# Kernel tuning notes

Measured on AMD Instinct MI355X. Metric: run time of the kernel, lower is better.

## Reference

```python
import jax, jax.numpy as jnp
import numpy as np

TOPK = 5    # top-k nearest neighbours for the loss
TOPKP = 10  # top-k' for the constraint mask


def _normalize(x):
    # matches torch F.normalize(dim=1) for well-conditioned random inputs
    return x / jnp.linalg.norm(x, axis=1, keepdims=True)


def setup_inputs() -> dict:
    key = jax.random.key(0)
    ks = jax.random.split(key, 9)
    B, D, K, N = 256, 512, 128000, 100000
    queue = _normalize(jax.random.normal(ks[2], (K, D), jnp.float32))  # init normalizes queue
    return {
        "query": jax.random.normal(ks[0], (B, D), jnp.float32),
        "current_target": jax.random.normal(ks[1], (B, D), jnp.float32),
        "queue": queue,
        "pool": jax.random.normal(ks[3], (2, N, D), jnp.float32),
        "labels_bank": jax.random.randint(ks[4], (B * 0 + K,), 0, 1000, dtype=jnp.int32).astype(jnp.int64) if False else jax.random.randint(ks[4], (K,), 0, 1000),
        "index_queue": jax.random.randint(ks[5], (K,), 0, N),
        "pool_qindex": jax.random.randint(ks[6], (N,), 0, 2),
        "labels": jax.random.randint(ks[7], (B,), 0, 1000),
        "indices": jax.random.randint(ks[8], (B,), 0, N),
    }


def reference(query, current_target, queue, pool, labels_bank, index_queue,
              pool_qindex, labels, indices):
    B = query.shape[0]
    q = _normalize(query)                                   # [B, D]
    # target branch is under torch.no_grad(); queue/pool are detached buffers
    t = jax.lax.stop_gradient(_normalize(current_target))   # [B, D]
    queue = jax.lax.stop_gradient(queue)
    pool = jax.lax.stop_gradient(pool)

    # --- _dequeue_and_enqueue with queue_ptr = 0 ---
    pool = pool.at[pool_qindex[indices], indices].set(t)
    pool_qindex = pool_qindex.at[indices].set((pool_qindex[indices] + 1) % 2)
    queue = queue.at[:B].set(t)
    labels_bank = labels_bank.at[:B].set(labels)
    index_queue = index_queue.at[:B].set(indices)

    # --- cdist (squared L2 of unit vectors) against the 128k bank ---
    dist_t = 2.0 - 2.0 * jnp.einsum('bc,kc->bk', t, queue)  # [B, K]
    dist_q = 2.0 - 2.0 * jnp.einsum('bc,kc->bk', q, queue)  # [B, K]

    # unconstrained NN: smallest distances == largest -dist
    _, un_idx = jax.lax.top_k(-dist_t, TOPK)                # [B, TOPK]
    nn_q_un = jnp.take_along_axis(dist_q, un_idx, axis=1)

    # --- constraint branch on the epoch pool ---
    targets_prime = pool[pool_qindex[index_queue], index_queue]  # [K, D]
    ct_prime = pool[pool_qindex[indices], indices]               # [B, D]
    dist_tp = 2.0 - 2.0 * jnp.einsum('bc,kc->bk', ct_prime, targets_prime)
    _, idx_p = jax.lax.top_k(-dist_tp, TOPKP)                    # [B, TOPKP]

    # scatter -5 at constrained positions (topk indices are unique, so add == set)
    dist_t = dist_t.at[jnp.arange(B)[:, None], idx_p].add(-5.0)

    _, con_idx = jax.lax.top_k(-dist_t, TOPK)
    nn_q_con = jnp.take_along_axis(dist_q, con_idx, axis=1)

    loss = ((nn_q_con.sum(axis=1) / TOPK).mean()
            + (nn_q_un.sum(axis=1) / TOPK).mean()) / 2.0

    matches = (labels_bank[un_idx] == labels[:, None]).astype(jnp.float32)
    purity = (matches.sum(axis=1) / TOPK).mean()
    return loss, purity
```

## Files before the change

### kernel.cpp

```cpp
#include <hip/hip_runtime.h>
#include <math.h>

#define B_SZ 256
#define D_SZ 512
#define K_SZ 128000
#define N_SZ 100000

#define OFF_T     0UL
#define OFF_Q     524288UL
#define OFF_TH    1048576UL
#define OFF_CTH   1310720UL
#define OFF_NPQ   1572864UL
#define OFF_TPROW 1973248UL
#define OFF_UN    2485248UL
#define OFF_IDXP  2490880UL
#define OFF_SC    2501632UL

typedef __attribute__((ext_vector_type(4))) float    f32x4;
typedef __attribute__((ext_vector_type(8))) _Float16 f16x8;

__device__ __forceinline__ float block_sum(float v, float* red) {
  #pragma unroll
  for (int o = 32; o > 0; o >>= 1) v += __shfl_down(v, o, 64);
  const int w = threadIdx.x >> 6;
  const int l = threadIdx.x & 63;
  __syncthreads();
  if (l == 0) red[w] = v;
  __syncthreads();
  return red[0] + red[1] + red[2] + red[3];
}

__global__ __launch_bounds__(256) void prep_rows_kernel(
    const float* __restrict__ query, const float* __restrict__ ctar,
    const float* __restrict__ pool, const int* __restrict__ pool_qindex,
    const int* __restrict__ indices,
    float* __restrict__ t_f32, float* __restrict__ q_f32,
    _Float16* __restrict__ t_f16, _Float16* __restrict__ ct_f16)
{
  __shared__ float red[4];
  const int b = blockIdx.x, tid = threadIdx.x;
  const long base = (long)b * D_SZ;
  float x0 = query[base + tid], x1 = query[base + 256 + tid];
  float y0 = ctar[base + tid],  y1 = ctar[base + 256 + tid];
  float sq = block_sum(x0 * x0 + x1 * x1, red);
  float st = block_sum(y0 * y0 + y1 * y1, red);
  float rq = 1.f / sqrtf(sq);
  float rt = 1.f / sqrtf(st);
  q_f32[base + tid] = x0 * rq; q_f32[base + 256 + tid] = x1 * rq;
  float t0 = y0 * rt, t1 = y1 * rt;
  t_f32[base + tid] = t0; t_f32[base + 256 + tid] = t1;
  t_f16[base + tid] = (_Float16)t0; t_f16[base + 256 + tid] = (_Float16)t1;
  int i = indices[b];
  int slot = 1 - pool_qindex[i];
  const float* pr = pool + ((long)slot * N_SZ + i) * D_SZ;
  ct_f16[base + tid] = (_Float16)pr[tid];
  ct_f16[base + 256 + tid] = (_Float16)pr[tid + 256];
}

__global__ void prep_newpq_kernel(const int* __restrict__ pq, int* __restrict__ new_pq) {
  int i = blockIdx.x * 256 + threadIdx.x;
  if (i < N_SZ) new_pq[i] = pq[i];
}

__global__ void prep_flip_kernel(const int* __restrict__ pq, const int* __restrict__ indices,
                                 int* __restrict__ new_pq) {
  int i = indices[threadIdx.x];
  new_pq[i] = 1 - pq[i];
}

__global__ void prep_tprow_kernel(const int* __restrict__ new_pq,
                                  const int* __restrict__ index_queue,
                                  const int* __restrict__ indices,
                                  int* __restrict__ tp_row) {
  int k = blockIdx.x * 256 + threadIdx.x;
  int i = (k < B_SZ) ? indices[k] : index_queue[k];
  tp_row[k] = new_pq[i] * N_SZ + i;
}

template<int MODE>
__global__ __launch_bounds__(256) void gemm_kernel(
    const float* __restrict__ queue, const float* __restrict__ pool,
    const float* __restrict__ t_f32, const _Float16* __restrict__ A_f16,
    const int* __restrict__ tp_row, float* __restrict__ scores)
{
  __shared__ __align__(16) _Float16 B_lds[64 * 72];
  const int tid  = threadIdx.x;
  const int lane = tid & 63;
  const int w    = tid >> 6;
  const int quad = lane >> 4;
  const int l15  = lane & 15;
  const long col0 = (long)blockIdx.x * 64;

  const int brow = tid >> 2;
  const int bch  = tid & 3;
  const long gcol = col0 + brow;
  const float* bsrc;
  if (MODE == 0) {
    bsrc = (gcol < B_SZ) ? (t_f32 + gcol * D_SZ) : (queue + gcol * D_SZ);
  } else {
    bsrc = pool + (long)tp_row[gcol] * D_SZ;
  }
  bsrc += bch * 16;

  f32x4 acc[4][4];
  #pragma unroll
  for (int mt = 0; mt < 4; ++mt)
    #pragma unroll
    for (int nt = 0; nt < 4; ++nt) acc[mt][nt] = (f32x4){0.f, 0.f, 0.f, 0.f};

  const _Float16* arow = A_f16 + (long)(w * 64 + l15) * D_SZ + quad * 8;

  #pragma unroll 1
  for (int kc = 0; kc < D_SZ; kc += 64) {
    float4 f0 = *(const float4*)(bsrc + kc + 0);
    float4 f1 = *(const float4*)(bsrc + kc + 4);
    float4 f2 = *(const float4*)(bsrc + kc + 8);
    float4 f3 = *(const float4*)(bsrc + kc + 12);
    f16x8 w0, w1;
    w0[0] = (_Float16)f0.x; w0[1] = (_Float16)f0.y; w0[2] = (_Float16)f0.z; w0[3] = (_Float16)f0.w;
    w0[4] = (_Float16)f1.x; w0[5] = (_Float16)f1.y; w0[6] = (_Float16)f1.z; w0[7] = (_Float16)f1.w;
    w1[0] = (_Float16)f2.x; w1[1] = (_Float16)f2.y; w1[2] = (_Float16)f2.z; w1[3] = (_Float16)f2.w;
    w1[4] = (_Float16)f3.x; w1[5] = (_Float16)f3.y; w1[6] = (_Float16)f3.z; w1[7] = (_Float16)f3.w;
    *(f16x8*)(&B_lds[brow * 72 + bch * 16])     = w0;
    *(f16x8*)(&B_lds[brow * 72 + bch * 16 + 8]) = w1;
    __syncthreads();
    #pragma unroll
    for (int ks = 0; ks < 2; ++ks) {
      f16x8 af[4], bfr[4];
      #pragma unroll
      for (int mt = 0; mt < 4; ++mt)
        af[mt] = *(const f16x8*)(arow + (long)mt * 16 * D_SZ + kc + ks * 32);
      #pragma unroll
      for (int nt = 0; nt < 4; ++nt)
        bfr[nt] = *(const f16x8*)(&B_lds[(nt * 16 + l15) * 72 + ks * 32 + quad * 8]);
      #pragma unroll
      for (int mt = 0; mt < 4; ++mt)
        #pragma unroll
        for (int nt = 0; nt < 4; ++nt)
          acc[mt][nt] = __builtin_amdgcn_mfma_f32_16x16x32_f16(af[mt], bfr[nt], acc[mt][nt], 0, 0, 0);
    }
    __syncthreads();
  }

  #pragma unroll
  for (int mt = 0; mt < 4; ++mt) {
    int row0 = w * 64 + mt * 16 + quad * 4;
    #pragma unroll
    for (int i = 0; i < 4; ++i) {
      long rbase = (long)(row0 + i) * K_SZ + col0;
      #pragma unroll
      for (int nt = 0; nt < 4; ++nt)
        scores[rbase + nt * 16 + l15] = acc[mt][nt][i];
    }
  }
}

template<int KS>
__global__ __launch_bounds__(256) void topk_kernel(
    const float* __restrict__ scores, int* __restrict__ out_idx)
{
  __shared__ float sv[256 * KS];
  __shared__ int   si[256 * KS];
  const int r = blockIdx.x;
  const int tid = threadIdx.x;
  float bv[KS]; int bi[KS];
  #pragma unroll
  for (int j = 0; j < KS; ++j) { bv[j] = -3.4e38f; bi[j] = 0x7fffffff; }
  const float4* srow = (const float4*)(scores + (long)r * K_SZ);
  for (int it = 0; it < K_SZ / 1024; ++it) {
    float4 v4 = srow[it * 256 + tid];
    int kb = (it * 256 + tid) * 4;
    float vv[4] = {v4.x, v4.y, v4.z, v4.w};
    #pragma unroll
    for (int j = 0; j < 4; ++j) {
      float v = vv[j];
      if (v > bv[KS - 1]) {
        bv[KS - 1] = v; bi[KS - 1] = kb + j;
        #pragma unroll
        for (int m = KS - 1; m > 0; --m) {
          if (bv[m] > bv[m - 1]) {
            float tv = bv[m]; bv[m] = bv[m - 1]; bv[m - 1] = tv;
            int   ti = bi[m]; bi[m] = bi[m - 1]; bi[m - 1] = ti;
          }
        }
      }
    }
  }
  #pragma unroll
  for (int j = 0; j < KS; ++j) { sv[tid * KS + j] = bv[j]; si[tid * KS + j] = bi[j]; }
  for (int s = 128; s > 0; s >>= 1) {
    __syncthreads();
    if (tid < s) {
      int pa = tid * KS, pb = (tid + s) * KS;
      float mv[KS]; int mi[KS];
      int ia = 0, ib = 0;
      #pragma unroll
      for (int j = 0; j < KS; ++j) {
        float va = sv[pa + ia], vb = sv[pb + ib];
        int   xa = si[pa + ia], xb = si[pb + ib];
        bool ta = (va > vb) || (va == vb && xa < xb);
        mv[j] = ta ? va : vb; mi[j] = ta ? xa : xb;
        if (ta) ++ia; else ++ib;
      }
      #pragma unroll
      for (int j = 0; j < KS; ++j) { sv[pa + j] = mv[j]; si[pa + j] = mi[j]; }
    }
  }
  __syncthreads();
  if (tid < KS) out_idx[r * KS + tid] = si[tid];
}

__global__ __launch_bounds__(256) void finalize_kernel(
    const float* __restrict__ t_f32, const float* __restrict__ q_f32,
    const float* __restrict__ queue,
    const int* __restrict__ un_idx, const int* __restrict__ idxp,
    const int* __restrict__ labels_bank, const int* __restrict__ labels,
    float* __restrict__ out)
{
  __shared__ float red[4];
  __shared__ float dvals[10];
  __shared__ int   csel[5];
  const int b = blockIdx.x;
  const int tid = threadIdx.x;
  const float* trow = t_f32 + (long)b * D_SZ;
  const float* qrow = q_f32 + (long)b * D_SZ;

  #pragma unroll 1
  for (int j = 0; j < 10; ++j) {
    int c = idxp[b * 10 + j];
    const float* cp = (c < B_SZ) ? (t_f32 + (long)c * D_SZ) : (queue + (long)c * D_SZ);
    float p = trow[tid] * cp[tid] + trow[tid + 256] * cp[tid + 256];
    float s = block_sum(p, red);
    if (tid == 0) dvals[j] = 2.f - 2.f * s;
  }
  __syncthreads();
  if (tid == 0) {
    unsigned used = 0;
    for (int m = 0; m < 5; ++m) {
      int best = -1; float bd = 0.f; int bc = 0;
      for (int j = 0; j < 10; ++j) {
        if (used & (1u << j)) continue;
        float dj = dvals[j]; int cj = idxp[b * 10 + j];
        if (best < 0 || dj < bd || (dj == bd && cj < bc)) { best = j; bd = dj; bc = cj; }
      }
      used |= 1u << best;
      csel[m] = idxp[b * 10 + best];
    }
  }
  __syncthreads();

  float con_s = 0.f, un_s = 0.f;
  #pragma unroll 1
  for (int m = 0; m < 5; ++m) {
    int c = csel[m];
    const float* cp = (c < B_SZ) ? (t_f32 + (long)c * D_SZ) : (queue + (long)c * D_SZ);
    float p = qrow[tid] * cp[tid] + qrow[tid + 256] * cp[tid + 256];
    con_s += block_sum(p, red);
  }
  int match = 0;
  #pragma unroll 1
  for (int m = 0; m < 5; ++m) {
    int c = un_idx[b * 5 + m];
    const float* cp = (c < B_SZ) ? (t_f32 + (long)c * D_SZ) : (queue + (long)c * D_SZ);
    float p = qrow[tid] * cp[tid] + qrow[tid + 256] * cp[tid + 256];
    un_s += block_sum(p, red);
    if (tid == 0) {
      int lb = (c < B_SZ) ? labels[c] : labels_bank[c];
      match += (lb == labels[b]) ? 1 : 0;
    }
  }
  if (tid == 0) {
    float con_sum = 10.f - 2.f * con_s;
    float un_sum  = 10.f - 2.f * un_s;
    float lossc = (con_sum * 0.2f + un_sum * 0.2f) * 0.5f * (1.f / 256.f);
    atomicAdd(out + 0, lossc);
    atomicAdd(out + 1, (float)match * 0.2f * (1.f / 256.f));
  }
}

extern "C" void kernel_launch(void* const* d_in, const int* in_sizes, int n_in,
                              void* d_out, int out_size, void* d_ws, size_t ws_size,
                              hipStream_t stream) {
  const float* query       = (const float*)d_in[0];
  const float* ctar        = (const float*)d_in[1];
  const float* queue       = (const float*)d_in[2];
  const float* pool        = (const float*)d_in[3];
  const int*   labels_bank = (const int*)d_in[4];
  const int*   index_queue = (const int*)d_in[5];
  const int*   pool_qindex = (const int*)d_in[6];
  const int*   labels      = (const int*)d_in[7];
  const int*   indices     = (const int*)d_in[8];

  char* ws = (char*)d_ws;
  float*     t_f32  = (float*)(ws + OFF_T);
  float*     q_f32  = (float*)(ws + OFF_Q);
  _Float16*  t_f16  = (_Float16*)(ws + OFF_TH);
  _Float16*  ct_f16 = (_Float16*)(ws + OFF_CTH);
  int*       new_pq = (int*)(ws + OFF_NPQ);
  int*       tp_row = (int*)(ws + OFF_TPROW);
  int*       un_idx = (int*)(ws + OFF_UN);
  int*       idxp   = (int*)(ws + OFF_IDXP);
  float*     scores = (float*)(ws + OFF_SC);
  float*     out    = (float*)d_out;

  hipMemsetAsync(out, 0, 2 * sizeof(float), stream);

  prep_rows_kernel<<<B_SZ, 256, 0, stream>>>(query, ctar, pool, pool_qindex, indices,
                                             t_f32, q_f32, t_f16, ct_f16);
  prep_newpq_kernel<<<(N_SZ + 255) / 256, 256, 0, stream>>>(pool_qindex, new_pq);
  prep_flip_kernel<<<1, 256, 0, stream>>>(pool_qindex, indices, new_pq);
  prep_tprow_kernel<<<K_SZ / 256, 256, 0, stream>>>(new_pq, index_queue, indices, tp_row);

  gemm_kernel<0><<<K_SZ / 64, 256, 0, stream>>>(queue, pool, t_f32, t_f16, tp_row, scores);
  topk_kernel<5><<<B_SZ, 256, 0, stream>>>(scores, un_idx);

  gemm_kernel<1><<<K_SZ / 64, 256, 0, stream>>>(queue, pool, t_f32, ct_f16, tp_row, scores);
  topk_kernel<10><<<B_SZ, 256, 0, stream>>>(scores, idxp);

  finalize_kernel<<<B_SZ, 256, 0, stream>>>(t_f32, q_f32, queue, un_idx, idxp,
                                            labels_bank, labels, out);
}
```

Measured before the change: 1.046 ms.

## Merge both score GEMMs and top-k passes into single launches with fp16 score buffers

The two GEMM launches become one grid of 4000 blocks that computes both branches, and the two top-k launches become one 512-block kernel. Scores are now stored as fp16 through an LDS transpose with 16-byte coalesced writes, halving the bytes written and re-read for the 256x128000 score matrices. The memset is folded into the prep kernel. The cost is more LDS per block, and fp16 score precision can change top-k ties or ordering, which risks picking different neighbours than the reference. The unconstrained branch now keeps a top-10 list and outputs its first 5 entries.

```diff
diff --git a/kernel.cpp b/kernel.cpp
--- a/kernel.cpp
+++ b/kernel.cpp
@@ -14,7 +14,8 @@
 #define OFF_TPROW 1973248UL
 #define OFF_UN    2485248UL
 #define OFF_IDXP  2490880UL
-#define OFF_SC    2501632UL
+#define OFF_SC0   2501632UL
+#define OFF_SC1   68037632UL
 
 typedef __attribute__((ext_vector_type(4))) float    f32x4;
 typedef __attribute__((ext_vector_type(8))) _Float16 f16x8;
@@ -35,10 +36,12 @@
     const float* __restrict__ pool, const int* __restrict__ pool_qindex,
     const int* __restrict__ indices,
     float* __restrict__ t_f32, float* __restrict__ q_f32,
-    _Float16* __restrict__ t_f16, _Float16* __restrict__ ct_f16)
+    _Float16* __restrict__ t_f16, _Float16* __restrict__ ct_f16,
+    float* __restrict__ out)
 {
   __shared__ float red[4];
   const int b = blockIdx.x, tid = threadIdx.x;
+  if (b == 0 && tid < 2) out[tid] = 0.f;
   const long base = (long)b * D_SZ;
   float x0 = query[base + tid], x1 = query[base + 256 + tid];
   float y0 = ctar[base + tid],  y1 = ctar[base + 256 + tid];
@@ -77,30 +80,31 @@
   tp_row[k] = new_pq[i] * N_SZ + i;
 }
 
-template<int MODE>
-__global__ __launch_bounds__(256) void gemm_kernel(
+__global__ __launch_bounds__(256) void gemm_fused_kernel(
     const float* __restrict__ queue, const float* __restrict__ pool,
-    const float* __restrict__ t_f32, const _Float16* __restrict__ A_f16,
-    const int* __restrict__ tp_row, float* __restrict__ scores)
+    const float* __restrict__ t_f32, const _Float16* __restrict__ t_f16,
+    const _Float16* __restrict__ ct_f16, const int* __restrict__ tp_row,
+    _Float16* __restrict__ sc0, _Float16* __restrict__ sc1)
 {
-  __shared__ __align__(16) _Float16 B_lds[64 * 72];
+  __shared__ __align__(16) _Float16 smem[4 * 64 * 72];
   const int tid  = threadIdx.x;
   const int lane = tid & 63;
   const int w    = tid >> 6;
   const int quad = lane >> 4;
   const int l15  = lane & 15;
-  const long col0 = (long)blockIdx.x * 64;
+  const bool br1 = blockIdx.x >= 2000;
+  const int  blk = br1 ? (blockIdx.x - 2000) : blockIdx.x;
+  const long col0 = (long)blk * 64;
 
   const int brow = tid >> 2;
   const int bch  = tid & 3;
   const long gcol = col0 + brow;
   const float* bsrc;
-  if (MODE == 0) {
-    bsrc = (gcol < B_SZ) ? (t_f32 + gcol * D_SZ) : (queue + gcol * D_SZ);
-  } else {
-    bsrc = pool + (long)tp_row[gcol] * D_SZ;
-  }
+  if (!br1) bsrc = (gcol < B_SZ) ? (t_f32 + gcol * D_SZ) : (queue + gcol * D_SZ);
+  else      bsrc = pool + (long)tp_row[gcol] * D_SZ;
   bsrc += bch * 16;
+
+  const _Float16* A_f16 = br1 ? ct_f16 : t_f16;
 
   f32x4 acc[4][4];
   #pragma unroll
@@ -121,8 +125,8 @@
     w0[4] = (_Float16)f1.x; w0[5] = (_Float16)f1.y; w0[6] = (_Float16)f1.z; w0[7] = (_Float16)f1.w;
     w1[0] = (_Float16)f2.x; w1[1] = (_Float16)f2.y; w1[2] = (_Float16)f2.z; w1[3] = (_Float16)f2.w;
     w1[4] = (_Float16)f3.x; w1[5] = (_Float16)f3.y; w1[6] = (_Float16)f3.z; w1[7] = (_Float16)f3.w;
-    *(f16x8*)(&B_lds[brow * 72 + bch * 16])     = w0;
-    *(f16x8*)(&B_lds[brow * 72 + bch * 16 + 8]) = w1;
+    *(f16x8*)(&smem[brow * 72 + bch * 16])     = w0;
+    *(f16x8*)(&smem[brow * 72 + bch * 16 + 8]) = w1;
     __syncthreads();
     #pragma unroll
     for (int ks = 0; ks < 2; ++ks) {
@@ -132,7 +136,7 @@
         af[mt] = *(const f16x8*)(arow + (long)mt * 16 * D_SZ + kc + ks * 32);
       #pragma unroll
       for (int nt = 0; nt < 4; ++nt)
-        bfr[nt] = *(const f16x8*)(&B_lds[(nt * 16 + l15) * 72 + ks * 32 + quad * 8]);
+        bfr[nt] = *(const f16x8*)(&smem[(nt * 16 + l15) * 72 + ks * 32 + quad * 8]);
       #pragma unroll
       for (int mt = 0; mt < 4; ++mt)
         #pragma unroll
@@ -142,42 +146,47 @@
     __syncthreads();
   }
 
-  #pragma unroll
-  for (int mt = 0; mt < 4; ++mt) {
-    int row0 = w * 64 + mt * 16 + quad * 4;
+  _Float16* outp = br1 ? sc1 : sc0;
+  _Float16* tb = smem + w * (64 * 72);
+  #pragma unroll
+  for (int mt = 0; mt < 4; ++mt)
     #pragma unroll
-    for (int i = 0; i < 4; ++i) {
-      long rbase = (long)(row0 + i) * K_SZ + col0;
-      #pragma unroll
-      for (int nt = 0; nt < 4; ++nt)
-        scores[rbase + nt * 16 + l15] = acc[mt][nt][i];
-    }
-  }
-}
-
-template<int KS>
-__global__ __launch_bounds__(256) void topk_kernel(
-    const float* __restrict__ scores, int* __restrict__ out_idx)
+    for (int nt = 0; nt < 4; ++nt)
+      #pragma unroll
+      for (int i = 0; i < 4; ++i)
+        tb[(mt * 16 + quad * 4 + i) * 72 + nt * 16 + l15] = (_Float16)acc[mt][nt][i];
+  #pragma unroll
+  for (int it = 0; it < 8; ++it) {
+    int lr = it * 8 + (lane >> 3);
+    int c  = lane & 7;
+    f16x8 v = *(const f16x8*)(tb + lr * 72 + c * 8);
+    *(f16x8*)(outp + (long)(w * 64 + lr) * K_SZ + col0 + c * 8) = v;
+  }
+}
+
+__global__ __launch_bounds__(256) void stage2_topk_kernel(
+    const _Float16* __restrict__ sc0, const _Float16* __restrict__ sc1,
+    int* __restrict__ un_idx, int* __restrict__ idxp)
 {
-  __shared__ float sv[256 * KS];
-  __shared__ int   si[256 * KS];
-  const int r = blockIdx.x;
-  const int tid = threadIdx.x;
-  float bv[KS]; int bi[KS];
-  #pragma unroll
-  for (int j = 0; j < KS; ++j) { bv[j] = -3.4e38f; bi[j] = 0x7fffffff; }
-  const float4* srow = (const float4*)(scores + (long)r * K_SZ);
-  for (int it = 0; it < K_SZ / 1024; ++it) {
-    float4 v4 = srow[it * 256 + tid];
-    int kb = (it * 256 + tid) * 4;
-    float vv[4] = {v4.x, v4.y, v4.z, v4.w};
+  __shared__ float sv[256 * 10];
+  __shared__ int   si[256 * 10];
+  const int  r   = blockIdx.x & 255;
+  const bool br1 = blockIdx.x >= 256;
+  const int  tid = threadIdx.x;
+  const _Float16* src = (br1 ? sc1 : sc0) + (long)r * K_SZ;
+  float bv[10]; int bi[10];
+  #pragma unroll
+  for (int j = 0; j < 10; ++j) { bv[j] = -3.4e38f; bi[j] = 0x7fffffff; }
+  for (int it = tid; it < K_SZ / 8; it += 256) {
+    f16x8 v8 = ((const f16x8*)src)[it];
+    int kb = it * 8;
     #pragma unroll
-    for (int j = 0; j < 4; ++j) {
-      float v = vv[j];
-      if (v > bv[KS - 1]) {
-        bv[KS - 1] = v; bi[KS - 1] = kb + j;
+    for (int j = 0; j < 8; ++j) {
+      float v = (float)v8[j];
+      if (v > bv[9]) {
+        bv[9] = v; bi[9] = kb + j;
         #pragma unroll
-        for (int m = KS - 1; m > 0; --m) {
+        for (int m = 9; m > 0; --m) {
           if (bv[m] > bv[m - 1]) {
             float tv = bv[m]; bv[m] = bv[m - 1]; bv[m - 1] = tv;
             int   ti = bi[m]; bi[m] = bi[m - 1]; bi[m - 1] = ti;
@@ -187,15 +196,15 @@
     }
   }
   #pragma unroll
-  for (int j = 0; j < KS; ++j) { sv[tid * KS + j] = bv[j]; si[tid * KS + j] = bi[j]; }
+  for (int j = 0; j < 10; ++j) { sv[tid * 10 + j] = bv[j]; si[tid * 10 + j] = bi[j]; }
   for (int s = 128; s > 0; s >>= 1) {
     __syncthreads();
     if (tid < s) {
-      int pa = tid * KS, pb = (tid + s) * KS;
-      float mv[KS]; int mi[KS];
+      int pa = tid * 10, pb = (tid + s) * 10;
+      float mv[10]; int mi[10];
       int ia = 0, ib = 0;
       #pragma unroll
-      for (int j = 0; j < KS; ++j) {
+      for (int j = 0; j < 10; ++j) {
         float va = sv[pa + ia], vb = sv[pb + ib];
         int   xa = si[pa + ia], xb = si[pb + ib];
         bool ta = (va > vb) || (va == vb && xa < xb);
@@ -203,11 +212,15 @@
         if (ta) ++ia; else ++ib;
       }
       #pragma unroll
-      for (int j = 0; j < KS; ++j) { sv[pa + j] = mv[j]; si[pa + j] = mi[j]; }
-    }
-  }
-  __syncthreads();
-  if (tid < KS) out_idx[r * KS + tid] = si[tid];
+      for (int j = 0; j < 10; ++j) { sv[pa + j] = mv[j]; si[pa + j] = mi[j]; }
+    }
+  }
+  __syncthreads();
+  if (tid < 10) {
+    int v = si[tid];
+    if (br1) idxp[r * 10 + tid] = v;
+    else if (tid < 5) un_idx[r * 5 + tid] = v;
+  }
 }
 
 __global__ __launch_bounds__(256) void finalize_kernel(
@@ -300,22 +313,19 @@
   int*       tp_row = (int*)(ws + OFF_TPROW);
   int*       un_idx = (int*)(ws + OFF_UN);
   int*       idxp   = (int*)(ws + OFF_IDXP);
-  float*     scores = (float*)(ws + OFF_SC);
+  _Float16*  sc0    = (_Float16*)(ws + OFF_SC0);
+  _Float16*  sc1    = (_Float16*)(ws + OFF_SC1);
   float*     out    = (float*)d_out;
 
-  hipMemsetAsync(out, 0, 2 * sizeof(float), stream);
-
   prep_rows_kernel<<<B_SZ, 256, 0, stream>>>(query, ctar, pool, pool_qindex, indices,
-                                             t_f32, q_f32, t_f16, ct_f16);
+                                             t_f32, q_f32, t_f16, ct_f16, out);
   prep_newpq_kernel<<<(N_SZ + 255) / 256, 256, 0, stream>>>(pool_qindex, new_pq);
   prep_flip_kernel<<<1, 256, 0, stream>>>(pool_qindex, indices, new_pq);
   prep_tprow_kernel<<<K_SZ / 256, 256, 0, stream>>>(new_pq, index_queue, indices, tp_row);
 
-  gemm_kernel<0><<<K_SZ / 64, 256, 0, stream>>>(queue, pool, t_f32, t_f16, tp_row, scores);
-  topk_kernel<5><<<B_SZ, 256, 0, stream>>>(scores, un_idx);
-
-  gemm_kernel<1><<<K_SZ / 64, 256, 0, stream>>>(queue, pool, t_f32, ct_f16, tp_row, scores);
-  topk_kernel<10><<<B_SZ, 256, 0, stream>>>(scores, idxp);
+  gemm_fused_kernel<<<2 * (K_SZ / 64), 256, 0, stream>>>(queue, pool, t_f32, t_f16, ct_f16,
+                                                         tp_row, sc0, sc1);
+  stage2_topk_kernel<<<512, 256, 0, stream>>>(sc0, sc1, un_idx, idxp);
 
   finalize_kernel<<<B_SZ, 256, 0, stream>>>(t_f32, q_f32, queue, un_idx, idxp,
                                             labels_bank, labels, out);
```

Measured after the change: 1.061 ms. Within noise of the previous version (+1.4%).
